# Performance work log

Measured on AMD Instinct MI355X. Metric: run time of the kernel, lower is better.

## Reference

```python
import jax, jax.numpy as jnp
import numpy as np

N = 100000
E = 1600000
D_IN = 128
D_HID = 128
D_OUT = 128
HEADS = 4
NEG_SLOPE = 0.2  # PyG GATConv default leaky_relu slope


def setup_inputs() -> dict:
    key = jax.random.key(0)
    ks = jax.random.split(key, 16)
    ch1 = D_HID // HEADS
    ch2 = D_OUT // HEADS
    inp = {
        "x": jax.random.normal(ks[0], (N, D_IN), dtype=jnp.float32),
        "edge_index": jax.random.randint(ks[1], (2, E), 0, N, dtype=jnp.int64),
        # conv1 params
        "W1": jax.random.normal(ks[2], (D_IN, HEADS * ch1), dtype=jnp.float32) * 0.05,
        "a1_src": jax.random.normal(ks[3], (HEADS, ch1), dtype=jnp.float32) * 0.05,
        "a1_dst": jax.random.normal(ks[4], (HEADS, ch1), dtype=jnp.float32) * 0.05,
        "b1": jnp.zeros((HEADS * ch1,), dtype=jnp.float32),
        # conv2 params
        "W2": jax.random.normal(ks[5], (D_HID, HEADS * ch2), dtype=jnp.float32) * 0.05,
        "a2_src": jax.random.normal(ks[6], (HEADS, ch2), dtype=jnp.float32) * 0.05,
        "a2_dst": jax.random.normal(ks[7], (HEADS, ch2), dtype=jnp.float32) * 0.05,
        "b2": jnp.zeros((HEADS * ch2,), dtype=jnp.float32),
        # residual linear
        "Wr": jax.random.normal(ks[8], (D_IN, D_OUT), dtype=jnp.float32) * 0.05,
        "br": jnp.zeros((D_OUT,), dtype=jnp.float32),
    }
    return inp


def _gat_conv(x, W, a_src, a_dst, bias, src, dst, n_nodes):
    """Single PyG-style GATConv (concat heads, eval-mode / no dropout).
    src/dst already include self loops. x: [N, Din]. Returns [N, H*C]."""
    H, C = a_src.shape
    h = (x @ W).reshape(n_nodes, H, C)                      # [N,H,C]
    s_src = jnp.einsum("nhc,hc->nh", h, a_src)              # [N,H]
    s_dst = jnp.einsum("nhc,hc->nh", h, a_dst)              # [N,H]
    e = s_src[src] + s_dst[dst]                             # [E',H]
    e = jnp.where(e > 0, e, NEG_SLOPE * e)                  # leaky_relu
    # softmax over edges grouped by destination node
    e_max = jax.ops.segment_max(e, dst, num_segments=n_nodes)  # [N,H]
    e_exp = jnp.exp(e - e_max[dst])
    denom = jax.ops.segment_sum(e_exp, dst, num_segments=n_nodes)  # [N,H]
    alpha = e_exp / denom[dst]                              # [E',H]
    msg = alpha[:, :, None] * h[src]                        # [E',H,C]
    out = jax.ops.segment_sum(msg, dst, num_segments=n_nodes)  # [N,H,C]
    return out.reshape(n_nodes, H * C) + bias


def reference(x, edge_index, W1, a1_src, a1_dst, b1, W2, a2_src, a2_dst, b2, Wr, br):
    n_nodes = x.shape[0]
    loops = jnp.arange(n_nodes, dtype=edge_index.dtype)
    src = jnp.concatenate([edge_index[0], loops])           # add_self_loops=True
    dst = jnp.concatenate([edge_index[1], loops])
    h1 = _gat_conv(x, W1, a1_src, a1_dst, b1, src, dst, n_nodes)
    h1 = jax.nn.relu(h1)
    h2 = _gat_conv(h1, W2, a2_src, a2_dst, b2, src, dst, n_nodes)
    return h2 + x @ Wr + br
```

## Files before the change

### kernel.cpp

```cpp
#include <hip/hip_runtime.h>

#define NEG_SLOPE 0.2f

__device__ __forceinline__ float leaky1(float e) { return e > 0.f ? e : NEG_SLOPE * e; }

__device__ __forceinline__ unsigned short f2bf(float f) {
    unsigned u = __float_as_uint(f);
    u += 0x7fffu + ((u >> 16) & 1u);
    return (unsigned short)(u >> 16);
}

#define EPB 4096

__global__ __launch_bounds__(256) void bucket_hist(const int* __restrict__ dst,
                                                   int* __restrict__ gcnt,
                                                   int* __restrict__ relBase,
                                                   int E, int N, int NB) {
    __shared__ int hist[256];
    int t = threadIdx.x, blk = blockIdx.x;
    if (t < NB) hist[t] = 0;
    __syncthreads();
    int e0 = blk * EPB + t;
#pragma unroll 4
    for (int k = 0; k < EPB / 256; ++k) {
        int e = e0 + k * 256;
        if (e < E) {
            int d = dst[e];
            if ((unsigned)d < (unsigned)N) atomicAdd(&hist[d >> 9], 1);
        }
    }
    __syncthreads();
    if (t < NB) relBase[blk * NB + t] = atomicAdd(&gcnt[t], hist[t]);
}

__global__ __launch_bounds__(256) void scan_buckets(const int* __restrict__ gcnt,
                                                    int* __restrict__ gboff, int NB) {
    __shared__ int sm[256];
    int t = threadIdx.x;
    int v = (t < NB) ? gcnt[t] : 0;
    sm[t] = v;
    __syncthreads();
#pragma unroll
    for (int o = 1; o < 256; o <<= 1) {
        int u = (t >= o) ? sm[t - o] : 0;
        __syncthreads();
        sm[t] += u;
        __syncthreads();
    }
    if (t < NB) gboff[t] = sm[t] - v;
    if (t == NB - 1) gboff[NB] = sm[t];
}

__global__ __launch_bounds__(256) void bucket_scatter(const int* __restrict__ src,
                                                      const int* __restrict__ dst,
                                                      const int* __restrict__ gboff,
                                                      const int* __restrict__ relBase,
                                                      int2* __restrict__ eb,
                                                      int E, int N, int NB) {
    __shared__ int cur[256];
    int t = threadIdx.x, blk = blockIdx.x;
    if (t < NB) cur[t] = gboff[t] + relBase[blk * NB + t];
    __syncthreads();
    int e0 = blk * EPB + t;
#pragma unroll 4
    for (int k = 0; k < EPB / 256; ++k) {
        int e = e0 + k * 256;
        if (e < E) {
            int d = dst[e];
            if ((unsigned)d < (unsigned)N) {
                int pos = atomicAdd(&cur[d >> 9], 1);
                eb[pos] = make_int2(src[e], d);
            }
        }
    }
}

__global__ __launch_bounds__(512) void csr_build(const int2* __restrict__ eb,
                                                 const int* __restrict__ gboff,
                                                 int* __restrict__ offs,
                                                 int* __restrict__ csr,
                                                 int N, int NB) {
    __shared__ int lcnt[512];
    __shared__ int sm[512];
    __shared__ int cur[512];
    int t = threadIdx.x, b = blockIdx.x;
    lcnt[t] = 0;
    __syncthreads();
    int s0 = gboff[b], s1 = gboff[b + 1];
    for (int e = s0 + t; e < s1; e += 512) atomicAdd(&lcnt[eb[e].y & 511], 1);
    __syncthreads();
    int v = lcnt[t];
    sm[t] = v;
    __syncthreads();
#pragma unroll
    for (int o = 1; o < 512; o <<= 1) {
        int u = (t >= o) ? sm[t - o] : 0;
        __syncthreads();
        sm[t] += u;
        __syncthreads();
    }
    int base = gboff[b] + sm[t] - v;
    cur[t] = base;
    int n0 = (b << 9) + t;
    if (n0 < N) offs[n0] = base;
    if (b == NB - 1 && t == 0) offs[N] = gboff[NB];
    __syncthreads();
    for (int e = s0 + t; e < s1; e += 512) {
        int2 p = eb[e];
        int pos = atomicAdd(&cur[p.y & 511], 1);
        csr[pos] = p.x;
    }
}


__global__ __launch_bounds__(256) void gemm128(const float* __restrict__ X,
                                               const float* __restrict__ W,
                                               float* __restrict__ OUT,
                                               unsigned short* __restrict__ HB,
                                               const float* __restrict__ bias,
                                               int accumulate,
                                               const float* __restrict__ ASrc,
                                               const float* __restrict__ ADst,
                                               float* __restrict__ sSt,
                                               float* __restrict__ sDt, int N) {
    __shared__ float Xs[32][128];
    __shared__ float Ws[64][128];
    int t = threadIdx.x;
    int row0 = blockIdx.x << 5;
    {
        const float4* xg = (const float4*)(X + (size_t)row0 * 128);
        float4* xs = (float4*)&Xs[0][0];
#pragma unroll
        for (int i = 0; i < 4; ++i) xs[t + 256 * i] = xg[t + 256 * i];
    }
    int cx = t & 31, ry = t >> 5;
    int c0 = cx << 2, r0 = ry << 2;
    float acc[4][4] = {};
#pragma unroll 1
    for (int ph = 0; ph < 2; ++ph) {
        __syncthreads();
        {
            const float4* wg = (const float4*)(W + (size_t)ph * 64 * 128);
            float4* ws = (float4*)&Ws[0][0];
#pragma unroll
            for (int i = 0; i < 8; ++i) ws[t + 256 * i] = wg[t + 256 * i];
        }
        __syncthreads();
#pragma unroll 4
        for (int k4 = 0; k4 < 16; ++k4) {
            float4 a[4], b[4];
#pragma unroll
            for (int i = 0; i < 4; ++i)
                a[i] = *(const float4*)&Xs[r0 + i][(ph << 6) + (k4 << 2)];
#pragma unroll
            for (int kk = 0; kk < 4; ++kk)
                b[kk] = *(const float4*)&Ws[(k4 << 2) + kk][c0];
#pragma unroll
            for (int i = 0; i < 4; ++i) {
                acc[i][0] = fmaf(a[i].x, b[0].x, acc[i][0]);
                acc[i][1] = fmaf(a[i].x, b[0].y, acc[i][1]);
                acc[i][2] = fmaf(a[i].x, b[0].z, acc[i][2]);
                acc[i][3] = fmaf(a[i].x, b[0].w, acc[i][3]);
                acc[i][0] = fmaf(a[i].y, b[1].x, acc[i][0]);
                acc[i][1] = fmaf(a[i].y, b[1].y, acc[i][1]);
                acc[i][2] = fmaf(a[i].y, b[1].z, acc[i][2]);
                acc[i][3] = fmaf(a[i].y, b[1].w, acc[i][3]);
                acc[i][0] = fmaf(a[i].z, b[2].x, acc[i][0]);
                acc[i][1] = fmaf(a[i].z, b[2].y, acc[i][1]);
                acc[i][2] = fmaf(a[i].z, b[2].z, acc[i][2]);
                acc[i][3] = fmaf(a[i].z, b[2].w, acc[i][3]);
                acc[i][0] = fmaf(a[i].w, b[3].x, acc[i][0]);
                acc[i][1] = fmaf(a[i].w, b[3].y, acc[i][1]);
                acc[i][2] = fmaf(a[i].w, b[3].z, acc[i][2]);
                acc[i][3] = fmaf(a[i].w, b[3].w, acc[i][3]);
            }
        }
    }
    float4 bv = make_float4(0.f, 0.f, 0.f, 0.f);
    if (bias) bv = *(const float4*)&bias[c0];
    float4 sa = make_float4(0.f, 0.f, 0.f, 0.f), da = sa;
    if (ASrc) {
        sa = *(const float4*)&ASrc[c0];
        da = *(const float4*)&ADst[c0];
    }
#pragma unroll
    for (int i = 0; i < 4; ++i) {
        size_t row = (size_t)(row0 + r0 + i);
        float4 o;
        o.x = acc[i][0] + bv.x;
        o.y = acc[i][1] + bv.y;
        o.z = acc[i][2] + bv.z;
        o.w = acc[i][3] + bv.w;
        if (accumulate) {
            const float4 old = *(const float4*)(OUT + row * 128 + c0);
            o.x += old.x; o.y += old.y; o.z += old.z; o.w += old.w;
        }
        if (OUT) *(float4*)(OUT + row * 128 + c0) = o;
        if (HB) {
            ushort4 hv;
            hv.x = f2bf(o.x); hv.y = f2bf(o.y); hv.z = f2bf(o.z); hv.w = f2bf(o.w);
            *(ushort4*)(HB + row * 128 + c0) = hv;
        }
        if (ASrc) {
            float ps = o.x * sa.x + o.y * sa.y + o.z * sa.z + o.w * sa.w;
            float pd = o.x * da.x + o.y * da.y + o.z * da.z + o.w * da.w;
            ps += __shfl_xor(ps, 1); pd += __shfl_xor(pd, 1);
            ps += __shfl_xor(ps, 2); pd += __shfl_xor(pd, 2);
            ps += __shfl_xor(ps, 4); pd += __shfl_xor(pd, 4);
            if ((cx & 7) == 0) {
                size_t sidx = (size_t)(cx >> 3) * N + row;
                sSt[sidx] = ps;
                sDt[sidx] = pd;
            }
        }
    }
}


__global__ __launch_bounds__(256) void agg5_kernel(const unsigned short* __restrict__ hb,
                                                   const float* __restrict__ sSt,
                                                   const float* __restrict__ sDt,
                                                   const int* __restrict__ offs,
                                                   const int* __restrict__ csr,
                                                   const float* __restrict__ bias,
                                                   float* __restrict__ out,
                                                   int do_relu, int N) {
    int n = (blockIdx.x << 2) + (threadIdx.x >> 6);
    if (n >= N) return;
    int lane = threadIdx.x & 63;
    int half = lane >> 5;
    int cl = lane & 31;
    int hd = cl >> 3;
    int whead = lane >> 4;
    int sub = lane & 15;

    size_t wb = (size_t)whead * N;
    float sdh = sDt[wb + n];
    float selfw = __expf(leaky1(sSt[wb + n] + sdh));

    float4 acc = make_float4(0.f, 0.f, 0.f, 0.f);
    float wsum = 0.f;

    int off = offs[n], end = offs[n + 1];
    for (int base = off; base < end; base += 64) {
        int idx = base + lane;
        int spre = (idx < end) ? csr[idx] : 0;
        int cnt = min(64, end - base);
#pragma unroll 1
        for (int lo = 0; lo < cnt; lo += 16) {
            float w = 0.f;
            {
                int s2 = __shfl(spre, lo + sub);
                if (lo + sub < cnt) w = __expf(leaky1(sSt[wb + s2] + sdh));
            }
            wsum += w;
#pragma unroll
            for (int i = 0; i < 16; i += 2) {
                int sj = __shfl(spre, lo + i + half);
                float wj = __shfl(w, (hd << 4) + i + half);
                uint2 v = *(const uint2*)(hb + (size_t)sj * 128 + 4 * cl);
                acc.x = fmaf(wj, __uint_as_float(v.x << 16), acc.x);
                acc.y = fmaf(wj, __uint_as_float(v.x & 0xffff0000u), acc.y);
                acc.z = fmaf(wj, __uint_as_float(v.y << 16), acc.z);
                acc.w = fmaf(wj, __uint_as_float(v.y & 0xffff0000u), acc.w);
            }
        }
    }
    acc.x += __shfl_xor(acc.x, 32);
    acc.y += __shfl_xor(acc.y, 32);
    acc.z += __shfl_xor(acc.z, 32);
    acc.w += __shfl_xor(acc.w, 32);
#pragma unroll
    for (int o = 8; o > 0; o >>= 1) wsum += __shfl_xor(wsum, o);
    float denom = wsum + selfw;
    float iv = 1.0f / __shfl(denom, hd << 4);
    float sw = __shfl(selfw, hd << 4);

    if (half == 0) {
        uint2 hv = *(const uint2*)(hb + (size_t)n * 128 + 4 * cl);
        float4 hs;
        hs.x = __uint_as_float(hv.x << 16);
        hs.y = __uint_as_float(hv.x & 0xffff0000u);
        hs.z = __uint_as_float(hv.y << 16);
        hs.w = __uint_as_float(hv.y & 0xffff0000u);
        float4 bvv = *(const float4*)(bias + 4 * cl);
        float4 o;
        o.x = fmaf(fmaf(sw, hs.x, acc.x), iv, bvv.x);
        o.y = fmaf(fmaf(sw, hs.y, acc.y), iv, bvv.y);
        o.z = fmaf(fmaf(sw, hs.z, acc.z), iv, bvv.z);
        o.w = fmaf(fmaf(sw, hs.w, acc.w), iv, bvv.w);
        if (do_relu) {
            o.x = fmaxf(o.x, 0.f); o.y = fmaxf(o.y, 0.f);
            o.z = fmaxf(o.z, 0.f); o.w = fmaxf(o.w, 0.f);
        }
        *(float4*)(out + (size_t)n * 128 + 4 * cl) = o;
    }
}


extern "C" void kernel_launch(void* const* d_in, const int* in_sizes, int n_in,
                              void* d_out, int out_size, void* d_ws, size_t ws_size,
                              hipStream_t stream) {
    const float* x   = (const float*)d_in[0];
    const int*   ei  = (const int*)d_in[1];
    const float* W1  = (const float*)d_in[2];
    const float* a1s = (const float*)d_in[3];
    const float* a1d = (const float*)d_in[4];
    const float* b1  = (const float*)d_in[5];
    const float* W2  = (const float*)d_in[6];
    const float* a2s = (const float*)d_in[7];
    const float* a2d = (const float*)d_in[8];
    const float* b2  = (const float*)d_in[9];
    const float* Wr  = (const float*)d_in[10];
    const float* br  = (const float*)d_in[11];
    float* out = (float*)d_out;

    int N = in_sizes[0] / 128;
    int E = in_sizes[1] / 2;
    const int* src = ei;
    const int* dst = ei + E;
    int NB = (N + 511) >> 9;
    int ebl = (E + EPB - 1) / EPB;

    char* w = (char*)d_ws;
    size_t p = 0;
    auto take = [&](size_t bytes) -> char* {
        char* r = w + p;
        p = (p + bytes + 255) & ~(size_t)255;
        return r;
    };
    float* bufB = (float*)take((size_t)N * 128 * 4);
    unsigned short* hb = (unsigned short*)take((size_t)N * 128 * 2);
    float* sSt  = (float*)take((size_t)N * 4 * 4);
    float* sDt  = (float*)take((size_t)N * 4 * 4);
    int* gcnt   = (int*)take((size_t)256 * 4);
    int* offs   = (int*)take((size_t)(N + 1) * 4);
    int* gboff  = (int*)take((size_t)257 * 4);
    int* relBase = (int*)take((size_t)ebl * NB * 4);
    int2* eb    = (int2*)take((size_t)E * 8);
    int* csr    = (int*)take((size_t)E * 4);

    hipMemsetAsync(gcnt, 0, 256 * 4, stream);

    bucket_hist<<<ebl, 256, 0, stream>>>(dst, gcnt, relBase, E, N, NB);
    scan_buckets<<<1, 256, 0, stream>>>(gcnt, gboff, NB);
    bucket_scatter<<<ebl, 256, 0, stream>>>(src, dst, gboff, relBase, eb, E, N, NB);
    csr_build<<<NB, 512, 0, stream>>>(eb, gboff, offs, csr, N, NB);

    int gb = N / 32;
    int ab = (N + 3) / 4;

    gemm128<<<gb, 256, 0, stream>>>(x, W1, nullptr, hb, nullptr, 0, a1s, a1d, sSt, sDt, N);
    agg5_kernel<<<ab, 256, 0, stream>>>(hb, sSt, sDt, offs, csr, b1, bufB, 1, N);
    gemm128<<<gb, 256, 0, stream>>>(bufB, W2, nullptr, hb, nullptr, 0, a2s, a2d, sSt, sDt, N);
    agg5_kernel<<<ab, 256, 0, stream>>>(hb, sSt, sDt, offs, csr, b2, out, 0, N);
    gemm128<<<gb, 256, 0, stream>>>(x, Wr, out, nullptr, br, 1, nullptr, nullptr, nullptr, nullptr, N);
}
```

Measured before the change: 490.4 us.

## Store attention scores node-major and compute edge weights per lane in aggregation

Attention score arrays change from head-major [H][N] to node-major [N][4], so one node's four head scores share a cache line. The aggregation kernel drops the shuffle-based sharing of indices and weights. Each lane now loads its 8 CSR indices and score values directly and computes its own exp weight, with redundant exp work across the 8 lanes of a head. Edges are processed 16 at a time with clamped index loads, and the per-head weight-sum reduction is simplified to a single cross-half shuffle.

Result: no change. 483.7 us (-1.4%).

```diff
diff --git a/kernel.cpp b/kernel.cpp
--- a/kernel.cpp
+++ b/kernel.cpp
@@ -121,8 +121,8 @@
                                                int accumulate,
                                                const float* __restrict__ ASrc,
                                                const float* __restrict__ ADst,
-                                               float* __restrict__ sSt,
-                                               float* __restrict__ sDt, int N) {
+                                               float* __restrict__ sS4,
+                                               float* __restrict__ sD4, int N) {
     __shared__ float Xs[32][128];
     __shared__ float Ws[64][128];
     int t = threadIdx.x;
@@ -208,18 +208,17 @@
             ps += __shfl_xor(ps, 2); pd += __shfl_xor(pd, 2);
             ps += __shfl_xor(ps, 4); pd += __shfl_xor(pd, 4);
             if ((cx & 7) == 0) {
-                size_t sidx = (size_t)(cx >> 3) * N + row;
-                sSt[sidx] = ps;
-                sDt[sidx] = pd;
+                sS4[row * 4 + (cx >> 3)] = ps;
+                sD4[row * 4 + (cx >> 3)] = pd;
             }
         }
     }
 }
 
 
-__global__ __launch_bounds__(256) void agg5_kernel(const unsigned short* __restrict__ hb,
-                                                   const float* __restrict__ sSt,
-                                                   const float* __restrict__ sDt,
+__global__ __launch_bounds__(256) void agg6_kernel(const unsigned short* __restrict__ hb,
+                                                   const float* __restrict__ sS4,
+                                                   const float* __restrict__ sD4,
                                                    const int* __restrict__ offs,
                                                    const int* __restrict__ csr,
                                                    const float* __restrict__ bias,
@@ -231,53 +230,52 @@
     int half = lane >> 5;
     int cl = lane & 31;
     int hd = cl >> 3;
-    int whead = lane >> 4;
-    int sub = lane & 15;
-
-    size_t wb = (size_t)whead * N;
-    float sdh = sDt[wb + n];
-    float selfw = __expf(leaky1(sSt[wb + n] + sdh));
+    unsigned clo = (unsigned)cl << 3;
+
+    float sdh = sD4[(n << 2) + hd];
+    float selfw = __expf(leaky1(sS4[(n << 2) + hd] + sdh));
 
     float4 acc = make_float4(0.f, 0.f, 0.f, 0.f);
     float wsum = 0.f;
 
     int off = offs[n], end = offs[n + 1];
-    for (int base = off; base < end; base += 64) {
-        int idx = base + lane;
-        int spre = (idx < end) ? csr[idx] : 0;
-        int cnt = min(64, end - base);
-#pragma unroll 1
-        for (int lo = 0; lo < cnt; lo += 16) {
-            float w = 0.f;
-            {
-                int s2 = __shfl(spre, lo + sub);
-                if (lo + sub < cnt) w = __expf(leaky1(sSt[wb + s2] + sdh));
-            }
+    for (int base = off; base < end; base += 16) {
+        int sj[8];
+        float wj[8];
+#pragma unroll
+        for (int i = 0; i < 8; ++i) {
+            int e = base + (i << 1) + half;
+            int ec = min(e, end - 1);
+            sj[i] = csr[ec];
+        }
+#pragma unroll
+        for (int i = 0; i < 8; ++i) {
+            int e = base + (i << 1) + half;
+            float s = sS4[((unsigned)sj[i] << 2) + hd] + sdh;
+            float w = __expf(leaky1(s));
+            wj[i] = (e < end) ? w : 0.f;
+        }
+#pragma unroll
+        for (int i = 0; i < 8; ++i) {
+            uint2 v = *(const uint2*)((const char*)hb + (((unsigned)sj[i] << 8) + clo));
+            float w = wj[i];
             wsum += w;
-#pragma unroll
-            for (int i = 0; i < 16; i += 2) {
-                int sj = __shfl(spre, lo + i + half);
-                float wj = __shfl(w, (hd << 4) + i + half);
-                uint2 v = *(const uint2*)(hb + (size_t)sj * 128 + 4 * cl);
-                acc.x = fmaf(wj, __uint_as_float(v.x << 16), acc.x);
-                acc.y = fmaf(wj, __uint_as_float(v.x & 0xffff0000u), acc.y);
-                acc.z = fmaf(wj, __uint_as_float(v.y << 16), acc.z);
-                acc.w = fmaf(wj, __uint_as_float(v.y & 0xffff0000u), acc.w);
-            }
+            acc.x = fmaf(w, __uint_as_float(v.x << 16), acc.x);
+            acc.y = fmaf(w, __uint_as_float(v.x & 0xffff0000u), acc.y);
+            acc.z = fmaf(w, __uint_as_float(v.y << 16), acc.z);
+            acc.w = fmaf(w, __uint_as_float(v.y & 0xffff0000u), acc.w);
         }
     }
     acc.x += __shfl_xor(acc.x, 32);
     acc.y += __shfl_xor(acc.y, 32);
     acc.z += __shfl_xor(acc.z, 32);
     acc.w += __shfl_xor(acc.w, 32);
-#pragma unroll
-    for (int o = 8; o > 0; o >>= 1) wsum += __shfl_xor(wsum, o);
-    float denom = wsum + selfw;
-    float iv = 1.0f / __shfl(denom, hd << 4);
-    float sw = __shfl(selfw, hd << 4);
+    wsum += __shfl_xor(wsum, 32);
+
+    float iv = 1.0f / (wsum + selfw);
 
     if (half == 0) {
-        uint2 hv = *(const uint2*)(hb + (size_t)n * 128 + 4 * cl);
+        uint2 hv = *(const uint2*)((const char*)hb + (((unsigned)n << 8) + clo));
         float4 hs;
         hs.x = __uint_as_float(hv.x << 16);
         hs.y = __uint_as_float(hv.x & 0xffff0000u);
@@ -285,10 +283,10 @@
         hs.w = __uint_as_float(hv.y & 0xffff0000u);
         float4 bvv = *(const float4*)(bias + 4 * cl);
         float4 o;
-        o.x = fmaf(fmaf(sw, hs.x, acc.x), iv, bvv.x);
-        o.y = fmaf(fmaf(sw, hs.y, acc.y), iv, bvv.y);
-        o.z = fmaf(fmaf(sw, hs.z, acc.z), iv, bvv.z);
-        o.w = fmaf(fmaf(sw, hs.w, acc.w), iv, bvv.w);
+        o.x = fmaf(fmaf(selfw, hs.x, acc.x), iv, bvv.x);
+        o.y = fmaf(fmaf(selfw, hs.y, acc.y), iv, bvv.y);
+        o.z = fmaf(fmaf(selfw, hs.z, acc.z), iv, bvv.z);
+        o.w = fmaf(fmaf(selfw, hs.w, acc.w), iv, bvv.w);
         if (do_relu) {
             o.x = fmaxf(o.x, 0.f); o.y = fmaxf(o.y, 0.f);
             o.z = fmaxf(o.z, 0.f); o.w = fmaxf(o.w, 0.f);
@@ -331,8 +329,8 @@
     };
     float* bufB = (float*)take((size_t)N * 128 * 4);
     unsigned short* hb = (unsigned short*)take((size_t)N * 128 * 2);
-    float* sSt  = (float*)take((size_t)N * 4 * 4);
-    float* sDt  = (float*)take((size_t)N * 4 * 4);
+    float* sS4  = (float*)take((size_t)N * 4 * 4);
+    float* sD4  = (float*)take((size_t)N * 4 * 4);
     int* gcnt   = (int*)take((size_t)256 * 4);
     int* offs   = (int*)take((size_t)(N + 1) * 4);
     int* gboff  = (int*)take((size_t)257 * 4);
@@ -350,9 +348,9 @@
     int gb = N / 32;
     int ab = (N + 3) / 4;
 
-    gemm128<<<gb, 256, 0, stream>>>(x, W1, nullptr, hb, nullptr, 0, a1s, a1d, sSt, sDt, N);
-    agg5_kernel<<<ab, 256, 0, stream>>>(hb, sSt, sDt, offs, csr, b1, bufB, 1, N);
-    gemm128<<<gb, 256, 0, stream>>>(bufB, W2, nullptr, hb, nullptr, 0, a2s, a2d, sSt, sDt, N);
-    agg5_kernel<<<ab, 256, 0, stream>>>(hb, sSt, sDt, offs, csr, b2, out, 0, N);
+    gemm128<<<gb, 256, 0, stream>>>(x, W1, nullptr, hb, nullptr, 0, a1s, a1d, sS4, sD4, N);
+    agg6_kernel<<<ab, 256, 0, stream>>>(hb, sS4, sD4, offs, csr, b1, bufB, 1, N);
+    gemm128<<<gb, 256, 0, stream>>>(bufB, W2, nullptr, hb, nullptr, 0, a2s, a2d, sS4, sD4, N);
+    agg6_kernel<<<ab, 256, 0, stream>>>(hb, sS4, sD4, offs, csr, b2, out, 0, N);
     gemm128<<<gb, 256, 0, stream>>>(x, Wr, out, nullptr, br, 1, nullptr, nullptr, nullptr, nullptr, N);
 }
```
